# Kernel optimization log

Measured on AMD Instinct MI355X. Metric: run time of the kernel, lower is better.

Reference implementation:

```python
import jax, jax.numpy as jnp
import numpy as np

B, D, NH, NT = 4096, 2048, 16, 4
DK = D // NH
EPS = 1e-5


def setup_inputs() -> dict:
    key = jax.random.key(0)
    ks = jax.random.split(key, 16)
    s = 0.02
    inp = {
        "e0": jax.random.normal(ks[0], (B, D), jnp.float32),
        "e1": jax.random.normal(ks[1], (B, D), jnp.float32),
        "e2": jax.random.normal(ks[2], (B, D), jnp.float32),
        "e3": jax.random.normal(ks[3], (B, D), jnp.float32),
        "quality": jax.random.uniform(ks[4], (B, NT), jnp.float32),
        "Wq": jax.random.normal(ks[5], (D, D), jnp.float32) * s,
        "bq": jnp.zeros((D,), jnp.float32),
        "Wk": jax.random.normal(ks[6], (D, D), jnp.float32) * s,
        "bk": jnp.zeros((D,), jnp.float32),
        "Wv": jax.random.normal(ks[7], (D, D), jnp.float32) * s,
        "bv": jnp.zeros((D,), jnp.float32),
        "Wo": jax.random.normal(ks[8], (D, D), jnp.float32) * s,
        "bo": jnp.zeros((D,), jnp.float32),
        "gamma": jnp.ones((D,), jnp.float32),
        "beta": jnp.zeros((D,), jnp.float32),
    }
    return inp


def _layer_norm(x, gamma, beta):
    mu = jnp.mean(x, axis=-1, keepdims=True)
    var = jnp.mean(jnp.square(x - mu), axis=-1, keepdims=True)
    return (x - mu) * jax.lax.rsqrt(var + EPS) * gamma + beta


def reference(e0, e1, e2, e3, quality, Wq, bq, Wk, bk, Wv, bv, Wo, bo, gamma, beta):
    # H: (B, T=4, D) stacked evidence representations
    H = jnp.stack([e0, e1, e2, e3], axis=1)
    # QKV projections, reshaped to (B, heads, T, dk)
    def proj(W, b):
        return (jnp.einsum('btd,ed->bte', H, W) + b).reshape(B, NT, NH, DK).transpose(0, 2, 1, 3)
    Q, K, V = proj(Wq, bq), proj(Wk, bk), proj(Wv, bv)
    # scores: (B, heads, Tq, Tk), scaled then multiplicatively quality-gated on keys
    scores = jnp.einsum('bhid,bhjd->bhij', Q, K) / jnp.sqrt(jnp.float32(DK))
    scores = scores * quality[:, None, None, :]
    attn = jax.nn.softmax(scores, axis=-1)  # dropout = identity at inference
    ctx = jnp.einsum('bhij,bhjd->bhid', attn, V)          # (B, H, T, dk)
    ctx = ctx.transpose(0, 2, 1, 3).reshape(B, NT, D)      # (B, T, D)
    ctx = jnp.einsum('btd,ed->bte', ctx, Wo) + bo
    fused = jnp.mean(ctx, axis=1)       # mean over evidence types
    residual = jnp.mean(H, axis=1)      # mean of ALL evidence types
    return _layer_norm(fused + residual, gamma, beta)
```

## Files before the change

### kernel.cpp

```cpp
#include <hip/hip_runtime.h>
#include <cstdint>
#include <cstddef>

#define BB 4096
#define DD 2048
#define NHH 16
#define NTT 4
#define DKK 128

using u16 = unsigned short;
using u32 = unsigned int;

typedef __bf16 bf16x8 __attribute__((ext_vector_type(8)));
typedef float f32x4 __attribute__((ext_vector_type(4)));

__device__ __forceinline__ float b2f(u16 u) {
    union { float f; u32 i; } c; c.i = ((u32)u) << 16; return c.f;
}
__device__ __forceinline__ u16 f2b(float f) {
    union { float f; u32 i; } c; c.f = f;
    u32 x = c.i;
    u32 r = (x + 0x7fffu + ((x >> 16) & 1u)) >> 16;
    return (u16)r;
}
__device__ __forceinline__ u32 pk(float lo, float hi) {
    u32 a = __builtin_bit_cast(u32, lo) + 0x8000u;
    u32 b = __builtin_bit_cast(u32, hi) + 0x8000u;
    return __builtin_amdgcn_perm(b, a, 0x07060302u);
}

__device__ __forceinline__ void load_lds16(const void* g, void* l) {
    __builtin_amdgcn_global_load_lds((const __attribute__((address_space(1))) void*)g,
                                     (__attribute__((address_space(3))) void*)l,
                                     16, 0, 0);
}

__global__ __launch_bounds__(256) void cvt_all(
    const float* __restrict__ e0, const float* __restrict__ e1,
    const float* __restrict__ e2, const float* __restrict__ e3,
    const float* __restrict__ Wq, const float* __restrict__ Wk,
    const float* __restrict__ Wv, const float* __restrict__ Wo,
    u16* __restrict__ Ebf, u16* __restrict__ W4)
{
    const int blk = blockIdx.x;
    const float* src;
    u16* dst;
    size_t i;
    if (blk < 16384) {
        const int t = blk & 3, b = blk >> 2;
        src = ((t == 0) ? e0 : (t == 1) ? e1 : (t == 2) ? e2 : e3) + (size_t)b * DD;
        dst = Ebf + (size_t)blk * DD;
        i = threadIdx.x * 8;
    } else {
        const int wb = blk - 16384;
        const int w = wb >> 11;
        src = (w == 0) ? Wq : (w == 1) ? Wk : (w == 2) ? Wv : Wo;
        dst = W4 + (size_t)w * DD * DD;
        i = (size_t)(wb & 2047) * 2048 + threadIdx.x * 8;
    }
    float4 a = *(const float4*)(src + i);
    float4 c = *(const float4*)(src + i + 4);
    *(uint4*)(dst + i) = make_uint4(pk(a.x, a.y), pk(a.z, a.w),
                                    pk(c.x, c.y), pk(c.z, c.w));
}

__global__ __launch_bounds__(256, 2) void qkv_attn(
    const u16* __restrict__ Ebf,
    const u16* __restrict__ Wqb, const u16* __restrict__ Wkb,
    const u16* __restrict__ Wvb,
    const float* __restrict__ bq, const float* __restrict__ bk,
    const float* __restrict__ bv, const float* __restrict__ qual,
    u16* __restrict__ ctx)
{
    __shared__ __align__(16) u16 As[128 * 32];
    __shared__ __align__(16) u16 BQs[128 * 32];
    __shared__ __align__(16) u16 BKs[128 * 32];
    __shared__ __align__(16) u16 BVs[128 * 32];

    const int tid = threadIdx.x;
    const int h = blockIdx.x;
    const int m0 = blockIdx.y * 128;
    const int n0 = h * 128;

    const int rs = tid >> 2;
    const int ks = (tid & 3) * 8;
    const u16* srcA1 = Ebf + (size_t)(m0 + rs) * DD + ks;
    const u16* srcA2 = srcA1 + (size_t)64 * DD;
    const u16* srcQ1 = Wqb + (size_t)(n0 + rs) * DD + ks;
    const u16* srcQ2 = srcQ1 + (size_t)64 * DD;
    const u16* srcK1 = Wkb + (size_t)(n0 + rs) * DD + ks;
    const u16* srcK2 = srcK1 + (size_t)64 * DD;
    const u16* srcV1 = Wvb + (size_t)(n0 + rs) * DD + ks;
    const u16* srcV2 = srcV1 + (size_t)64 * DD;

    const int wave = tid >> 6;
    char* ldsA1 = (char*)As  + wave * 1024;
    char* ldsA2 = (char*)As  + 4096 + wave * 1024;
    char* ldsQ1 = (char*)BQs + wave * 1024;
    char* ldsQ2 = (char*)BQs + 4096 + wave * 1024;
    char* ldsK1 = (char*)BKs + wave * 1024;
    char* ldsK2 = (char*)BKs + 4096 + wave * 1024;
    char* ldsV1 = (char*)BVs + wave * 1024;
    char* ldsV2 = (char*)BVs + 4096 + wave * 1024;

    const int lane = tid & 63;
    const int lrow = lane & 15;
    const int lk = (lane >> 4) * 8;
    const int wm = wave * 32;

    f32x4 aQ[2][8] = {};
    f32x4 aK[2][8] = {};
    f32x4 aV[2][8] = {};

    for (int k0 = 0; k0 < DD; k0 += 32) {
        __syncthreads();
        load_lds16(srcA1, ldsA1);
        load_lds16(srcA2, ldsA2);
        load_lds16(srcQ1, ldsQ1);
        load_lds16(srcQ2, ldsQ2);
        load_lds16(srcK1, ldsK1);
        load_lds16(srcK2, ldsK2);
        load_lds16(srcV1, ldsV1);
        load_lds16(srcV2, ldsV2);
        srcA1 += 32; srcA2 += 32; srcQ1 += 32; srcQ2 += 32;
        srcK1 += 32; srcK2 += 32; srcV1 += 32; srcV2 += 32;
        __syncthreads();

        bf16x8 af0 = *(const bf16x8*)(As + (wm + lrow) * 32 + lk);
        bf16x8 af1 = *(const bf16x8*)(As + (wm + 16 + lrow) * 32 + lk);
#pragma unroll
        for (int ni = 0; ni < 8; ++ni) {
            const int boff = (ni * 16 + lrow) * 32 + lk;
            bf16x8 bqf = *(const bf16x8*)(BQs + boff);
            bf16x8 bkf = *(const bf16x8*)(BKs + boff);
            bf16x8 bvf = *(const bf16x8*)(BVs + boff);
            aQ[0][ni] = __builtin_amdgcn_mfma_f32_16x16x32_bf16(af0, bqf, aQ[0][ni], 0, 0, 0);
            aQ[1][ni] = __builtin_amdgcn_mfma_f32_16x16x32_bf16(af1, bqf, aQ[1][ni], 0, 0, 0);
            aK[0][ni] = __builtin_amdgcn_mfma_f32_16x16x32_bf16(af0, bkf, aK[0][ni], 0, 0, 0);
            aK[1][ni] = __builtin_amdgcn_mfma_f32_16x16x32_bf16(af1, bkf, aK[1][ni], 0, 0, 0);
            aV[0][ni] = __builtin_amdgcn_mfma_f32_16x16x32_bf16(af0, bvf, aV[0][ni], 0, 0, 0);
            aV[1][ni] = __builtin_amdgcn_mfma_f32_16x16x32_bf16(af1, bvf, aV[1][ni], 0, 0, 0);
        }
    }

    const int quad = lane >> 4;
    const int lcol = lane & 15;

    float qb[8], kb[8], vb[8];
#pragma unroll
    for (int ni = 0; ni < 8; ++ni) {
        const int col = n0 + ni * 16 + lcol;
        qb[ni] = bq[col]; kb[ni] = bk[col]; vb[ni] = bv[col];
    }

#pragma unroll
    for (int mi = 0; mi < 2; ++mi) {
        const int bbat = (m0 >> 2) + wave * 8 + mi * 4 + quad;

        float ps[4][4];
#pragma unroll
        for (int t = 0; t < 4; ++t)
#pragma unroll
            for (int j = 0; j < 4; ++j) ps[t][j] = 0.f;

#pragma unroll
        for (int ni = 0; ni < 8; ++ni) {
            float qv[4], kv[4];
#pragma unroll
            for (int t = 0; t < 4; ++t) {
                qv[t] = aQ[mi][ni][t] + qb[ni];
                kv[t] = aK[mi][ni][t] + kb[ni];
            }
#pragma unroll
            for (int t = 0; t < 4; ++t)
#pragma unroll
                for (int j = 0; j < 4; ++j) ps[t][j] += qv[t] * kv[j];
        }
#pragma unroll
        for (int t = 0; t < 4; ++t)
#pragma unroll
            for (int j = 0; j < 4; ++j) {
                ps[t][j] += __shfl_xor(ps[t][j], 1);
                ps[t][j] += __shfl_xor(ps[t][j], 2);
                ps[t][j] += __shfl_xor(ps[t][j], 4);
                ps[t][j] += __shfl_xor(ps[t][j], 8);
            }

        const float scale = 0.08838834764831845f;
        float qj[4];
#pragma unroll
        for (int j = 0; j < 4; ++j) qj[j] = qual[bbat * 4 + j] * scale;

        float wsum[4] = {0.f, 0.f, 0.f, 0.f};
#pragma unroll
        for (int t = 0; t < 4; ++t) {
            float sm[4]; float mx = -1e30f;
#pragma unroll
            for (int j = 0; j < 4; ++j) { sm[j] = ps[t][j] * qj[j]; mx = fmaxf(mx, sm[j]); }
            float ex[4]; float se = 0.f;
#pragma unroll
            for (int j = 0; j < 4; ++j) { ex[j] = __expf(sm[j] - mx); se += ex[j]; }
            const float inv = 0.25f / se;
#pragma unroll
            for (int j = 0; j < 4; ++j) wsum[j] += ex[j] * inv;
        }

#pragma unroll
        for (int ni = 0; ni < 8; ++ni) {
            const int col = n0 + ni * 16 + lcol;
            float r = wsum[0] * aV[mi][ni][0] + wsum[1] * aV[mi][ni][1]
                    + wsum[2] * aV[mi][ni][2] + wsum[3] * aV[mi][ni][3] + vb[ni];
            ctx[(size_t)bbat * DD + col] = f2b(r);
        }
    }
}

__global__ __launch_bounds__(256) void o_gemm(
    const u16* __restrict__ A, const u16* __restrict__ W,
    const float* __restrict__ bia, float* __restrict__ Y)
{
    __shared__ __align__(16) u16 As[128 * 32];
    __shared__ __align__(16) u16 Bs[128 * 32];

    const int tid = threadIdx.x;
    const int m0 = blockIdx.x * 128;
    const int n0 = blockIdx.y * 128;

    const int rs = tid >> 2;
    const int ks = (tid & 3) * 8;
    const u16* srcA1 = A + (size_t)(m0 + rs) * DD + ks;
    const u16* srcA2 = srcA1 + (size_t)64 * DD;
    const u16* srcB1 = W + (size_t)(n0 + rs) * DD + ks;
    const u16* srcB2 = srcB1 + (size_t)64 * DD;

    const int wave = tid >> 6;
    char* ldsA1 = (char*)As + wave * 1024;
    char* ldsA2 = (char*)As + 4096 + wave * 1024;
    char* ldsB1 = (char*)Bs + wave * 1024;
    char* ldsB2 = (char*)Bs + 4096 + wave * 1024;

    const int lane = tid & 63;
    const int wm = (wave >> 1) * 64;
    const int wn = (wave & 1) * 64;
    const int lrow = lane & 15;
    const int lk = (lane >> 4) * 8;

    f32x4 acc[4][4] = {};

    for (int k0 = 0; k0 < DD; k0 += 32) {
        __syncthreads();
        load_lds16(srcA1, ldsA1);
        load_lds16(srcA2, ldsA2);
        load_lds16(srcB1, ldsB1);
        load_lds16(srcB2, ldsB2);
        srcA1 += 32; srcA2 += 32; srcB1 += 32; srcB2 += 32;
        __syncthreads();

        bf16x8 af[4], bfr[4];
#pragma unroll
        for (int i = 0; i < 4; ++i)
            af[i] = *(const bf16x8*)(As + (wm + i * 16 + lrow) * 32 + lk);
#pragma unroll
        for (int i = 0; i < 4; ++i)
            bfr[i] = *(const bf16x8*)(Bs + (wn + i * 16 + lrow) * 32 + lk);
#pragma unroll
        for (int mi = 0; mi < 4; ++mi)
#pragma unroll
            for (int ni = 0; ni < 4; ++ni)
                acc[mi][ni] = __builtin_amdgcn_mfma_f32_16x16x32_bf16(af[mi], bfr[ni], acc[mi][ni], 0, 0, 0);
    }

#pragma unroll
    for (int mi = 0; mi < 4; ++mi) {
#pragma unroll
        for (int r = 0; r < 4; ++r) {
            const int grow = m0 + wm + mi * 16 + (lane >> 4) * 4 + r;
#pragma unroll
            for (int ni = 0; ni < 4; ++ni) {
                const int gcol = n0 + wn + ni * 16 + (lane & 15);
                Y[(size_t)grow * DD + gcol] = acc[mi][ni][r] + bia[gcol];
            }
        }
    }
}

__global__ __launch_bounds__(256) void ln_kernel(
    const float* __restrict__ Y,
    const float* __restrict__ e0, const float* __restrict__ e1,
    const float* __restrict__ e2, const float* __restrict__ e3,
    const float* __restrict__ gamma, const float* __restrict__ beta,
    float* __restrict__ out)
{
    const int r = blockIdx.x;
    const int tid = threadIdx.x;
    const int c = tid * 8;
    const size_t base = (size_t)r * DD + c;

    float v[8];
    {
        float4 y0 = *(const float4*)(Y + base);
        float4 y1 = *(const float4*)(Y + base + 4);
        float a[8] = {0, 0, 0, 0, 0, 0, 0, 0};
        const float* eps[4] = {e0, e1, e2, e3};
#pragma unroll
        for (int qq = 0; qq < 4; ++qq) {
            float4 p0 = *(const float4*)(eps[qq] + base);
            float4 p1 = *(const float4*)(eps[qq] + base + 4);
            a[0] += p0.x; a[1] += p0.y; a[2] += p0.z; a[3] += p0.w;
            a[4] += p1.x; a[5] += p1.y; a[6] += p1.z; a[7] += p1.w;
        }
        float yv[8] = {y0.x, y0.y, y0.z, y0.w, y1.x, y1.y, y1.z, y1.w};
#pragma unroll
        for (int i = 0; i < 8; ++i) v[i] = yv[i] + 0.25f * a[i];
    }

    float s = 0.f, sq = 0.f;
#pragma unroll
    for (int i = 0; i < 8; ++i) { s += v[i]; sq += v[i] * v[i]; }
#pragma unroll
    for (int off = 32; off >= 1; off >>= 1) {
        s += __shfl_xor(s, off);
        sq += __shfl_xor(sq, off);
    }
    __shared__ float sh[8];
    const int lane = tid & 63, wv = tid >> 6;
    if (lane == 0) { sh[wv] = s; sh[4 + wv] = sq; }
    __syncthreads();
    s = sh[0] + sh[1] + sh[2] + sh[3];
    sq = sh[4] + sh[5] + sh[6] + sh[7];

    const float invD = 1.0f / 2048.0f;
    const float mu = s * invD;
    const float rs = rsqrtf(sq * invD - mu * mu + 1e-5f);

    float4 g0 = *(const float4*)(gamma + c);
    float4 g1 = *(const float4*)(gamma + c + 4);
    float4 b0 = *(const float4*)(beta + c);
    float4 b1 = *(const float4*)(beta + c + 4);
    float gg[8] = {g0.x, g0.y, g0.z, g0.w, g1.x, g1.y, g1.z, g1.w};
    float bb[8] = {b0.x, b0.y, b0.z, b0.w, b1.x, b1.y, b1.z, b1.w};

    float o[8];
#pragma unroll
    for (int i = 0; i < 8; ++i) o[i] = (v[i] - mu) * rs * gg[i] + bb[i];
    *(float4*)(out + base)     = make_float4(o[0], o[1], o[2], o[3]);
    *(float4*)(out + base + 4) = make_float4(o[4], o[5], o[6], o[7]);
}

extern "C" void kernel_launch(void* const* d_in, const int* in_sizes, int n_in,
                              void* d_out, int out_size, void* d_ws, size_t ws_size,
                              hipStream_t stream)
{
    const float* e0   = (const float*)d_in[0];
    const float* e1   = (const float*)d_in[1];
    const float* e2   = (const float*)d_in[2];
    const float* e3   = (const float*)d_in[3];
    const float* qual = (const float*)d_in[4];
    const float* Wq   = (const float*)d_in[5];
    const float* bq   = (const float*)d_in[6];
    const float* Wk   = (const float*)d_in[7];
    const float* bk   = (const float*)d_in[8];
    const float* Wv   = (const float*)d_in[9];
    const float* bv   = (const float*)d_in[10];
    const float* Wo   = (const float*)d_in[11];
    const float* bo   = (const float*)d_in[12];
    const float* gm   = (const float*)d_in[13];
    const float* bt   = (const float*)d_in[14];

    const size_t WD = (size_t)DD * DD;
    const size_t MQ = (size_t)BB * NTT * DD;
    const size_t ED = (size_t)BB * DD;

    u16* Ebf = (u16*)d_ws;
    u16* W4  = Ebf + MQ;
    u16* ctx = W4 + 4 * WD;
    float* Y = (float*)(ctx + ED);

    cvt_all<<<dim3(24576), 256, 0, stream>>>(e0, e1, e2, e3, Wq, Wk, Wv, Wo,
                                             Ebf, W4);

    qkv_attn<<<dim3(16, 128), 256, 0, stream>>>(Ebf, W4, W4 + WD, W4 + 2 * WD,
                                                bq, bk, bv, qual, ctx);

    o_gemm<<<dim3(32, 16), 256, 0, stream>>>(ctx, W4 + 3 * WD, bo, Y);

    ln_kernel<<<dim3(4096), 256, 0, stream>>>(Y, e0, e1, e2, e3, gm, bt,
                                              (float*)d_out);
}
```

Baseline: 689.1 us.

## Double K-tile depth to 64 with XOR-swizzled LDS layout in both GEMMs

Both the fused QKV-attention kernel and the output-projection GEMM now stage 64-wide K slices per iteration instead of 32. This halves the number of barrier pairs and global-to-LDS load rounds. Source columns are XOR-swizzled by row on load, and fragment reads use the matching XOR offset, to avoid LDS bank conflicts on the wider 128-byte rows. LDS use doubles, which may reduce occupancy, notably for qkv_attn which now needs 64KB per block with launch bounds asking for 2 blocks.

```diff
diff --git a/kernel.cpp b/kernel.cpp
--- a/kernel.cpp
+++ b/kernel.cpp
@@ -72,74 +72,74 @@
     const float* __restrict__ bv, const float* __restrict__ qual,
     u16* __restrict__ ctx)
 {
-    __shared__ __align__(16) u16 As[128 * 32];
-    __shared__ __align__(16) u16 BQs[128 * 32];
-    __shared__ __align__(16) u16 BKs[128 * 32];
-    __shared__ __align__(16) u16 BVs[128 * 32];
+    __shared__ __align__(16) u16 As [128 * 64];
+    __shared__ __align__(16) u16 BQs[128 * 64];
+    __shared__ __align__(16) u16 BKs[128 * 64];
+    __shared__ __align__(16) u16 BVs[128 * 64];
 
     const int tid = threadIdx.x;
     const int h = blockIdx.x;
     const int m0 = blockIdx.y * 128;
     const int n0 = h * 128;
 
-    const int rs = tid >> 2;
-    const int ks = (tid & 3) * 8;
-    const u16* srcA1 = Ebf + (size_t)(m0 + rs) * DD + ks;
-    const u16* srcA2 = srcA1 + (size_t)64 * DD;
-    const u16* srcQ1 = Wqb + (size_t)(n0 + rs) * DD + ks;
-    const u16* srcQ2 = srcQ1 + (size_t)64 * DD;
-    const u16* srcK1 = Wkb + (size_t)(n0 + rs) * DD + ks;
-    const u16* srcK2 = srcK1 + (size_t)64 * DD;
-    const u16* srcV1 = Wvb + (size_t)(n0 + rs) * DD + ks;
-    const u16* srcV2 = srcV1 + (size_t)64 * DD;
-
     const int wave = tid >> 6;
-    char* ldsA1 = (char*)As  + wave * 1024;
-    char* ldsA2 = (char*)As  + 4096 + wave * 1024;
-    char* ldsQ1 = (char*)BQs + wave * 1024;
-    char* ldsQ2 = (char*)BQs + 4096 + wave * 1024;
-    char* ldsK1 = (char*)BKs + wave * 1024;
-    char* ldsK2 = (char*)BKs + 4096 + wave * 1024;
-    char* ldsV1 = (char*)BVs + wave * 1024;
-    char* ldsV2 = (char*)BVs + 4096 + wave * 1024;
-
     const int lane = tid & 63;
+
+    const int srow = wave * 8 + (lane >> 3);
+    const int scol = ((lane & 7) ^ (lane >> 3)) * 8;
+    const u16* srcA = Ebf + (size_t)(m0 + srow) * DD + scol;
+    const u16* srcQ = Wqb + (size_t)(n0 + srow) * DD + scol;
+    const u16* srcK = Wkb + (size_t)(n0 + srow) * DD + scol;
+    const u16* srcV = Wvb + (size_t)(n0 + srow) * DD + scol;
+
+    char* ldsA = (char*)As  + wave * 1024;
+    char* ldsQ = (char*)BQs + wave * 1024;
+    char* ldsK = (char*)BKs + wave * 1024;
+    char* ldsV = (char*)BVs + wave * 1024;
+
     const int lrow = lane & 15;
-    const int lk = (lane >> 4) * 8;
+    const int q4 = lane >> 4;
     const int wm = wave * 32;
+    const int soff0 = (q4 ^ (lrow & 7)) * 16;
+    const int aoff0 = (wm + lrow) * 128;
+    const int aoff1 = aoff0 + 16 * 128;
+    const int boffr = lrow * 128;
 
     f32x4 aQ[2][8] = {};
     f32x4 aK[2][8] = {};
     f32x4 aV[2][8] = {};
 
-    for (int k0 = 0; k0 < DD; k0 += 32) {
+    for (int k0 = 0; k0 < DD; k0 += 64) {
         __syncthreads();
-        load_lds16(srcA1, ldsA1);
-        load_lds16(srcA2, ldsA2);
-        load_lds16(srcQ1, ldsQ1);
-        load_lds16(srcQ2, ldsQ2);
-        load_lds16(srcK1, ldsK1);
-        load_lds16(srcK2, ldsK2);
-        load_lds16(srcV1, ldsV1);
-        load_lds16(srcV2, ldsV2);
-        srcA1 += 32; srcA2 += 32; srcQ1 += 32; srcQ2 += 32;
-        srcK1 += 32; srcK2 += 32; srcV1 += 32; srcV2 += 32;
+#pragma unroll
+        for (int i = 0; i < 4; ++i) {
+            const size_t go = (size_t)i * 32 * DD;
+            load_lds16(srcA + go, ldsA + i * 4096);
+            load_lds16(srcQ + go, ldsQ + i * 4096);
+            load_lds16(srcK + go, ldsK + i * 4096);
+            load_lds16(srcV + go, ldsV + i * 4096);
+        }
+        srcA += 64; srcQ += 64; srcK += 64; srcV += 64;
         __syncthreads();
 
-        bf16x8 af0 = *(const bf16x8*)(As + (wm + lrow) * 32 + lk);
-        bf16x8 af1 = *(const bf16x8*)(As + (wm + 16 + lrow) * 32 + lk);
-#pragma unroll
-        for (int ni = 0; ni < 8; ++ni) {
-            const int boff = (ni * 16 + lrow) * 32 + lk;
-            bf16x8 bqf = *(const bf16x8*)(BQs + boff);
-            bf16x8 bkf = *(const bf16x8*)(BKs + boff);
-            bf16x8 bvf = *(const bf16x8*)(BVs + boff);
-            aQ[0][ni] = __builtin_amdgcn_mfma_f32_16x16x32_bf16(af0, bqf, aQ[0][ni], 0, 0, 0);
-            aQ[1][ni] = __builtin_amdgcn_mfma_f32_16x16x32_bf16(af1, bqf, aQ[1][ni], 0, 0, 0);
-            aK[0][ni] = __builtin_amdgcn_mfma_f32_16x16x32_bf16(af0, bkf, aK[0][ni], 0, 0, 0);
-            aK[1][ni] = __builtin_amdgcn_mfma_f32_16x16x32_bf16(af1, bkf, aK[1][ni], 0, 0, 0);
-            aV[0][ni] = __builtin_amdgcn_mfma_f32_16x16x32_bf16(af0, bvf, aV[0][ni], 0, 0, 0);
-            aV[1][ni] = __builtin_amdgcn_mfma_f32_16x16x32_bf16(af1, bvf, aV[1][ni], 0, 0, 0);
+#pragma unroll
+        for (int kk = 0; kk < 2; ++kk) {
+            const int so = soff0 ^ (kk * 64);
+            bf16x8 af0 = *(const bf16x8*)((const char*)As + aoff0 + so);
+            bf16x8 af1 = *(const bf16x8*)((const char*)As + aoff1 + so);
+#pragma unroll
+            for (int ni = 0; ni < 8; ++ni) {
+                const int boff = boffr + ni * 16 * 128 + so;
+                bf16x8 bqf = *(const bf16x8*)((const char*)BQs + boff);
+                bf16x8 bkf = *(const bf16x8*)((const char*)BKs + boff);
+                bf16x8 bvf = *(const bf16x8*)((const char*)BVs + boff);
+                aQ[0][ni] = __builtin_amdgcn_mfma_f32_16x16x32_bf16(af0, bqf, aQ[0][ni], 0, 0, 0);
+                aQ[1][ni] = __builtin_amdgcn_mfma_f32_16x16x32_bf16(af1, bqf, aQ[1][ni], 0, 0, 0);
+                aK[0][ni] = __builtin_amdgcn_mfma_f32_16x16x32_bf16(af0, bkf, aK[0][ni], 0, 0, 0);
+                aK[1][ni] = __builtin_amdgcn_mfma_f32_16x16x32_bf16(af1, bkf, aK[1][ni], 0, 0, 0);
+                aV[0][ni] = __builtin_amdgcn_mfma_f32_16x16x32_bf16(af0, bvf, aV[0][ni], 0, 0, 0);
+                aV[1][ni] = __builtin_amdgcn_mfma_f32_16x16x32_bf16(af1, bvf, aV[1][ni], 0, 0, 0);
+            }
         }
     }
 
@@ -219,55 +219,59 @@
     const u16* __restrict__ A, const u16* __restrict__ W,
     const float* __restrict__ bia, float* __restrict__ Y)
 {
-    __shared__ __align__(16) u16 As[128 * 32];
-    __shared__ __align__(16) u16 Bs[128 * 32];
+    __shared__ __align__(16) u16 As[128 * 64];
+    __shared__ __align__(16) u16 Bs[128 * 64];
 
     const int tid = threadIdx.x;
     const int m0 = blockIdx.x * 128;
     const int n0 = blockIdx.y * 128;
 
-    const int rs = tid >> 2;
-    const int ks = (tid & 3) * 8;
-    const u16* srcA1 = A + (size_t)(m0 + rs) * DD + ks;
-    const u16* srcA2 = srcA1 + (size_t)64 * DD;
-    const u16* srcB1 = W + (size_t)(n0 + rs) * DD + ks;
-    const u16* srcB2 = srcB1 + (size_t)64 * DD;
-
     const int wave = tid >> 6;
-    char* ldsA1 = (char*)As + wave * 1024;
-    char* ldsA2 = (char*)As + 4096 + wave * 1024;
-    char* ldsB1 = (char*)Bs + wave * 1024;
-    char* ldsB2 = (char*)Bs + 4096 + wave * 1024;
-
     const int lane = tid & 63;
+
+    const int srow = wave * 8 + (lane >> 3);
+    const int scol = ((lane & 7) ^ (lane >> 3)) * 8;
+    const u16* srcA = A + (size_t)(m0 + srow) * DD + scol;
+    const u16* srcB = W + (size_t)(n0 + srow) * DD + scol;
+
+    char* ldsA = (char*)As + wave * 1024;
+    char* ldsB = (char*)Bs + wave * 1024;
+
     const int wm = (wave >> 1) * 64;
     const int wn = (wave & 1) * 64;
     const int lrow = lane & 15;
-    const int lk = (lane >> 4) * 8;
+    const int q4 = lane >> 4;
+    const int soff0 = (q4 ^ (lrow & 7)) * 16;
 
     f32x4 acc[4][4] = {};
 
-    for (int k0 = 0; k0 < DD; k0 += 32) {
+    for (int k0 = 0; k0 < DD; k0 += 64) {
         __syncthreads();
-        load_lds16(srcA1, ldsA1);
-        load_lds16(srcA2, ldsA2);
-        load_lds16(srcB1, ldsB1);
-        load_lds16(srcB2, ldsB2);
-        srcA1 += 32; srcA2 += 32; srcB1 += 32; srcB2 += 32;
+#pragma unroll
+        for (int i = 0; i < 4; ++i) {
+            const size_t go = (size_t)i * 32 * DD;
+            load_lds16(srcA + go, ldsA + i * 4096);
+            load_lds16(srcB + go, ldsB + i * 4096);
+        }
+        srcA += 64; srcB += 64;
         __syncthreads();
 
-        bf16x8 af[4], bfr[4];
-#pragma unroll
-        for (int i = 0; i < 4; ++i)
-            af[i] = *(const bf16x8*)(As + (wm + i * 16 + lrow) * 32 + lk);
-#pragma unroll
-        for (int i = 0; i < 4; ++i)
-            bfr[i] = *(const bf16x8*)(Bs + (wn + i * 16 + lrow) * 32 + lk);
-#pragma unroll
-        for (int mi = 0; mi < 4; ++mi)
-#pragma unroll
-            for (int ni = 0; ni < 4; ++ni)
-                acc[mi][ni] = __builtin_amdgcn_mfma_f32_16x16x32_bf16(af[mi], bfr[ni], acc[mi][ni], 0, 0, 0);
+#pragma unroll
+        for (int kk = 0; kk < 2; ++kk) {
+            const int so = soff0 ^ (kk * 64);
+            bf16x8 af[4], bfr[4];
+#pragma unroll
+            for (int i = 0; i < 4; ++i)
+                af[i] = *(const bf16x8*)((const char*)As + (wm + i * 16 + lrow) * 128 + so);
+#pragma unroll
+            for (int i = 0; i < 4; ++i)
+                bfr[i] = *(const bf16x8*)((const char*)Bs + (wn + i * 16 + lrow) * 128 + so);
+#pragma unroll
+            for (int mi = 0; mi < 4; ++mi)
+#pragma unroll
+                for (int ni = 0; ni < 4; ++ni)
+                    acc[mi][ni] = __builtin_amdgcn_mfma_f32_16x16x32_bf16(af[mi], bfr[ni], acc[mi][ni], 0, 0, 0);
+        }
     }
 
 #pragma unroll
```

Measured after the change: 641.8 us. 6.9% less time.
